# Performance work log

Measured on AMD Instinct MI355X. Metric: run time of the kernel, lower is better.

The kernel has to match this reference:

```python
import jax, jax.numpy as jnp
import numpy as np

N, E, CIN, COUT = 100000, 1600000, 64, 128
EPS = 1e-5  # torch BatchNorm default


def setup_inputs() -> dict:
    key = jax.random.key(0)
    ks = jax.random.split(key, 16)
    s = 0.1
    x = jax.random.normal(ks[0], (N, CIN), jnp.float32)
    src = jax.random.randint(ks[1], (E,), 0, N, dtype=jnp.int32)
    dst = jax.random.randint(ks[2], (E,), 0, N, dtype=jnp.int32)
    edge_index = jnp.stack([src, dst])  # [2, E]
    return {
        "x": x,
        "edge_index": edge_index,
        # conv0: GraphConv(CIN -> COUT)
        "W_root0": jax.random.normal(ks[3], (COUT, CIN), jnp.float32) * s,
        "W_nbr0": jax.random.normal(ks[4], (COUT, CIN), jnp.float32) * s,
        "b0": jnp.zeros((COUT,), jnp.float32),
        # bn0
        "g0": jnp.ones((COUT,), jnp.float32),
        "be0": jnp.zeros((COUT,), jnp.float32),
        # conv1: GraphConv(COUT -> COUT)
        "W_root1": jax.random.normal(ks[5], (COUT, COUT), jnp.float32) * s,
        "W_nbr1": jax.random.normal(ks[6], (COUT, COUT), jnp.float32) * s,
        "b1": jnp.zeros((COUT,), jnp.float32),
        # bn1
        "g1": jnp.ones((COUT,), jnp.float32),
        "be1": jnp.zeros((COUT,), jnp.float32),
        # residual 1x1 conv (Conv1d(CIN, COUT, 1))
        "Wlin": jax.random.normal(ks[7], (COUT, CIN), jnp.float32) * s,
        "blin": jnp.zeros((COUT,), jnp.float32),
    }


def graph_conv(x, src, dst, W_root, W_nbr, b):
    # PyG GraphConv: out_i = W_root x_i + W_nbr * sum_{j: (j->i) in E} x_j + b
    agg = jax.ops.segment_sum(x[src], dst, num_segments=N)  # scatter-add over edges
    return x @ W_root.T + agg @ W_nbr.T + b


def batch_norm(x, gamma, beta):
    # training-mode BatchNorm over the node dimension (biased variance)
    mu = jnp.mean(x, axis=0)
    var = jnp.mean(jnp.square(x - mu), axis=0)
    return (x - mu) * jax.lax.rsqrt(var + EPS) * gamma + beta


def reference(x, edge_index, W_root0, W_nbr0, b0, g0, be0,
              W_root1, W_nbr1, b1, g1, be1, Wlin, blin):
    src, dst = edge_index[0], edge_index[1]
    y = batch_norm(graph_conv(x, src, dst, W_root0, W_nbr0, b0), g0, be0)
    y = jax.nn.relu(y)
    y = batch_norm(graph_conv(y, src, dst, W_root1, W_nbr1, b1), g1, be1)
    out = y + (x @ Wlin.T + blin)  # 1x1 Conv1d residual projection
    return jax.nn.relu(out)
```

## Files before the change

kernel.cpp:

```cpp
#include <hip/hip_runtime.h>
#include <stdint.h>


#define CIN 64
#define COUT 128
#define BN_EPS 1e-5f
#define CURPAD 32
#define PCPAD 32
#define SPAD 32
#define PSH 8
#define PNODES (1 << PSH)
#define MAXP 512

typedef unsigned short u16;
typedef short short8 __attribute__((ext_vector_type(8)));
typedef float f32x4 __attribute__((ext_vector_type(4)));

__device__ __forceinline__ float bf2f(u16 u) {
    union { unsigned int i; float f; } v; v.i = ((unsigned int)u) << 16; return v.f;
}
__device__ __forceinline__ u16 f2bf(float f) {
    union { float f; unsigned int i; } v; v.f = f;
    unsigned int r = v.i + 0x7fffu + ((v.i >> 16) & 1u);
    return (u16)(r >> 16);
}
__device__ __forceinline__ float lo16(unsigned int w) { return bf2f((u16)(w & 0xffffu)); }
__device__ __forceinline__ float hi16(unsigned int w) { return bf2f((u16)(w >> 16)); }

template<bool BF> __device__ __forceinline__ float ldf(const void* p, long i) {
    if (BF) return bf2f(((const u16*)p)[i]);
    return ((const float*)p)[i];
}
template<bool BF> __device__ __forceinline__ short8 ld8(const void* p, long i) {
    if (BF) return *(const short8*)((const u16*)p + i);
    const float* f = (const float*)p + i;
    short8 r;
#pragma unroll
    for (int j = 0; j < 8; ++j) r[j] = (short)f2bf(f[j]);
    return r;
}

__device__ __forceinline__ void acc8(float* a, uint4 w) {
    a[0] += lo16(w.x); a[1] += hi16(w.x);
    a[2] += lo16(w.y); a[3] += hi16(w.y);
    a[4] += lo16(w.z); a[5] += hi16(w.z);
    a[6] += lo16(w.w); a[7] += hi16(w.w);
}

__global__ void k_detect(const unsigned int* __restrict__ x, int* __restrict__ flag) {
    int lane = threadIdx.x;
    int cnt = 0;
#pragma unroll
    for (int i = 0; i < 8; ++i) {
        unsigned int w = x[lane * 8 + i];
        unsigned int e0 = (w >> 7) & 0xFFu, e1 = (w >> 23) & 0xFFu;
        cnt += (e0 >= 0x60u && e0 <= 0x8Eu);
        cnt += (e1 >= 0x60u && e1 <= 0x8Eu);
    }
    for (int o = 32; o; o >>= 1) cnt += __shfl_down(cnt, o);
    if (lane == 0) *flag = (cnt > 850) ? 1 : 0;
}

__global__ __launch_bounds__(256) void k_xbf(const int* __restrict__ flag,
        const void* __restrict__ x, u16* __restrict__ xb, long n8) {
    long idx = (long)blockIdx.x * 256 + threadIdx.x;
    long stride = (long)gridDim.x * 256;
    uint4* dst = (uint4*)xb;
    if (*flag) {
        const uint4* src = (const uint4*)x;
        for (; idx < n8; idx += stride) dst[idx] = src[idx];
    } else {
        const float4* src = (const float4*)x;
        for (; idx < n8; idx += stride) {
            float4 a = src[idx * 2], b = src[idx * 2 + 1];
            uint4 o;
            o.x = (unsigned int)f2bf(a.x) | ((unsigned int)f2bf(a.y) << 16);
            o.y = (unsigned int)f2bf(a.z) | ((unsigned int)f2bf(a.w) << 16);
            o.z = (unsigned int)f2bf(b.x) | ((unsigned int)f2bf(b.y) << 16);
            o.w = (unsigned int)f2bf(b.z) | ((unsigned int)f2bf(b.w) << 16);
            dst[idx] = o;
        }
    }
}

__global__ __launch_bounds__(256) void k_phist(const int* __restrict__ dst,
                                               int* __restrict__ pcount, int E, int np) {
    __shared__ int h[MAXP];
    for (int i = threadIdx.x; i < np; i += 256) h[i] = 0;
    __syncthreads();
    int stride = gridDim.x * 256;
    for (int e = blockIdx.x * 256 + threadIdx.x; e < E; e += stride)
        atomicAdd(&h[dst[e] >> PSH], 1);
    __syncthreads();
    for (int i = threadIdx.x; i < np; i += 256)
        if (h[i]) atomicAdd(&pcount[i * PCPAD], h[i]);
}

__global__ void k_pscan(const int* __restrict__ pcount, int* __restrict__ pstart,
                        int* __restrict__ pcursor, int np, int E) {
    __shared__ int s[MAXP];
    int t = threadIdx.x;
    int v = (t < np) ? pcount[t * PCPAD] : 0;
    s[t] = v; __syncthreads();
    for (int o = 1; o < MAXP; o <<= 1) {
        int u = (t >= o) ? s[t - o] : 0;
        __syncthreads(); s[t] += u; __syncthreads();
    }
    if (t < np) {
        int ex = s[t] - v;
        pstart[t] = ex;
        pcursor[t * CURPAD] = ex;
    }
    if (t == 0) pstart[np] = E;
}

__global__ __launch_bounds__(256) void k_pfill(const int* __restrict__ src,
        const int* __restrict__ dst, int* __restrict__ pcursor,
        unsigned int* __restrict__ barr, int E, int np) {
    __shared__ int cnt[MAXP], gb[MAXP], loc[MAXP];
    int tid = threadIdx.x;
    int base = blockIdx.x * 4096;
    for (int i = tid; i < np; i += 256) { cnt[i] = 0; loc[i] = 0; }
    __syncthreads();
    int pk[16]; unsigned int rec[16];
#pragma unroll
    for (int k = 0; k < 16; ++k) {
        int e = base + k * 256 + tid;
        if (e < E) {
            int d = dst[e];
            pk[k] = d >> PSH;
            rec[k] = ((unsigned int)(d & (PNODES - 1)) << 20) | (unsigned int)src[e];
            atomicAdd(&cnt[pk[k]], 1);
        } else pk[k] = -1;
    }
    __syncthreads();
    for (int i = tid; i < np; i += 256)
        if (cnt[i]) gb[i] = atomicAdd(&pcursor[i * CURPAD], cnt[i]);
    __syncthreads();
#pragma unroll
    for (int k = 0; k < 16; ++k) {
        if (pk[k] >= 0) {
            int off = atomicAdd(&loc[pk[k]], 1);
            barr[gb[pk[k]] + off] = rec[k];
        }
    }
}

__global__ __launch_bounds__(256) void k_psort(const unsigned int* __restrict__ barr,
        const int* __restrict__ pstart, int* __restrict__ csr,
        int* __restrict__ row_start, int n, int np, int E) {
    __shared__ int hist[PNODES], curs[PNODES], tsum[256];
    int tid = threadIdx.x;
    int p = blockIdx.x;
    int e0 = pstart[p], e1 = pstart[p + 1];
    int node0 = p << PSH;
    hist[tid] = 0;
    __syncthreads();
    for (int t = e0 + tid; t < e1; t += 256)
        atomicAdd(&hist[barr[t] >> 20], 1);
    __syncthreads();
    int v = hist[tid];
    tsum[tid] = v; __syncthreads();
    for (int o = 1; o < 256; o <<= 1) {
        int u = (tid >= o) ? tsum[tid - o] : 0;
        __syncthreads(); tsum[tid] += u; __syncthreads();
    }
    int ex = tsum[tid] - v;
    curs[tid] = ex;
    int nd = node0 + tid;
    if (nd < n) row_start[nd] = e0 + ex;
    if (p == np - 1 && tid == 0) row_start[n] = E;
    __syncthreads();
    for (int t = e0 + tid; t < e1; t += 256) {
        unsigned int rec = barr[t];
        int pos = atomicAdd(&curs[rec >> 20], 1);
        csr[e0 + pos] = (int)(rec & 0xFFFFF);
    }
}

__global__ __launch_bounds__(256) void k_agg0(const u16* __restrict__ xb,
        const int* __restrict__ rs, const int* __restrict__ csr,
        u16* __restrict__ agg, int n) {
    int i = blockIdx.x * 4 + (threadIdx.x >> 6);
    if (i >= n) return;
    int lane = threadIdx.x & 63;
    int slot = lane >> 4, cp = lane & 15;
    const unsigned int* x32 = (const unsigned int*)xb;
    int b = rs[i], e = rs[i + 1];
    float acc[4] = {0.f, 0.f, 0.f, 0.f};
    int t = b + slot;
    for (; t + 12 < e; t += 16) {
        int j0 = csr[t], j1 = csr[t + 4], j2 = csr[t + 8], j3 = csr[t + 12];
        uint2 w0 = *((const uint2*)(x32 + (long)j0 * 32) + cp);
        uint2 w1 = *((const uint2*)(x32 + (long)j1 * 32) + cp);
        uint2 w2 = *((const uint2*)(x32 + (long)j2 * 32) + cp);
        uint2 w3 = *((const uint2*)(x32 + (long)j3 * 32) + cp);
        acc[0] += lo16(w0.x) + lo16(w1.x); acc[1] += hi16(w0.x) + hi16(w1.x);
        acc[2] += lo16(w0.y) + lo16(w1.y); acc[3] += hi16(w0.y) + hi16(w1.y);
        acc[0] += lo16(w2.x) + lo16(w3.x); acc[1] += hi16(w2.x) + hi16(w3.x);
        acc[2] += lo16(w2.y) + lo16(w3.y); acc[3] += hi16(w2.y) + hi16(w3.y);
    }
    for (; t < e; t += 4) {
        int j0 = csr[t];
        uint2 w0 = *((const uint2*)(x32 + (long)j0 * 32) + cp);
        acc[0] += lo16(w0.x); acc[1] += hi16(w0.x);
        acc[2] += lo16(w0.y); acc[3] += hi16(w0.y);
    }
#pragma unroll
    for (int k = 0; k < 4; ++k) {
        acc[k] += __shfl_xor(acc[k], 16);
        acc[k] += __shfl_xor(acc[k], 32);
    }
    if (slot == 0) {
        uint2 o;
        o.x = (unsigned int)f2bf(acc[0]) | ((unsigned int)f2bf(acc[1]) << 16);
        o.y = (unsigned int)f2bf(acc[2]) | ((unsigned int)f2bf(acc[3]) << 16);
        *((uint2*)((unsigned int*)agg + (long)i * 32) + cp) = o;
    }
}

__global__ __launch_bounds__(256) void k_y0p(unsigned int* __restrict__ y0,
        const float* __restrict__ sc, const float* __restrict__ sh, long nq) {
    long idx = (long)blockIdx.x * 256 + threadIdx.x;
    int colq = threadIdx.x & 15;
    float s8[8], h8[8];
#pragma unroll
    for (int j = 0; j < 8; ++j) { s8[j] = sc[colq * 8 + j]; h8[j] = sh[colq * 8 + j]; }
    long stride = (long)gridDim.x * 256;
    uint4* p = (uint4*)y0;
    for (; idx < nq; idx += stride) {
        uint4 w = p[idx];
        unsigned int r[4] = {w.x, w.y, w.z, w.w};
        uint4 o;
        unsigned int* po = (unsigned int*)&o;
#pragma unroll
        for (int d = 0; d < 4; ++d) {
            float a = fmaxf(lo16(r[d]) * s8[2 * d]     + h8[2 * d],     0.f);
            float b = fmaxf(hi16(r[d]) * s8[2 * d + 1] + h8[2 * d + 1], 0.f);
            po[d] = (unsigned int)f2bf(a) | ((unsigned int)f2bf(b) << 16);
        }
        p[idx] = o;
    }
}

__global__ __launch_bounds__(256) void k_agg1(const u16* __restrict__ y0p,
        const int* __restrict__ rs, const int* __restrict__ csr,
        u16* __restrict__ agg, int n) {
    int i = blockIdx.x * 4 + (threadIdx.x >> 6);
    if (i >= n) return;
    int lane = threadIdx.x & 63;
    int slot = lane >> 4, cp = lane & 15;
    const unsigned int* y32 = (const unsigned int*)y0p;
    int b = rs[i], e = rs[i + 1];
    float acc[8] = {0.f, 0.f, 0.f, 0.f, 0.f, 0.f, 0.f, 0.f};
    int t = b + slot;
    for (; t + 12 < e; t += 16) {
        int j0 = csr[t], j1 = csr[t + 4], j2 = csr[t + 8], j3 = csr[t + 12];
        uint4 w0 = *((const uint4*)(y32 + (long)j0 * 64) + cp);
        uint4 w1 = *((const uint4*)(y32 + (long)j1 * 64) + cp);
        uint4 w2 = *((const uint4*)(y32 + (long)j2 * 64) + cp);
        uint4 w3 = *((const uint4*)(y32 + (long)j3 * 64) + cp);
        acc8(acc, w0); acc8(acc, w1); acc8(acc, w2); acc8(acc, w3);
    }
    for (; t < e; t += 4) {
        int j0 = csr[t];
        uint4 w0 = *((const uint4*)(y32 + (long)j0 * 64) + cp);
        acc8(acc, w0);
    }
#pragma unroll
    for (int k = 0; k < 8; ++k) {
        acc[k] += __shfl_xor(acc[k], 16);
        acc[k] += __shfl_xor(acc[k], 32);
    }
    if (slot == 0) {
        uint4 o;
        o.x = (unsigned int)f2bf(acc[0]) | ((unsigned int)f2bf(acc[1]) << 16);
        o.y = (unsigned int)f2bf(acc[2]) | ((unsigned int)f2bf(acc[3]) << 16);
        o.z = (unsigned int)f2bf(acc[4]) | ((unsigned int)f2bf(acc[5]) << 16);
        o.w = (unsigned int)f2bf(acc[6]) | ((unsigned int)f2bf(acc[7]) << 16);
        *((uint4*)((unsigned int*)agg + (long)i * 64) + cp) = o;
    }
}

template<bool BF>
__device__ __forceinline__ void gemm0_impl(const u16* xb, const u16* agg,
                                           const void* Wr, const void* Wn,
                                           u16* y0, float* sumP, float* sqP,
                                           int n, int nch) {
    int tid = threadIdx.x;
    int wave = tid >> 6, lane = tid & 63, lr = lane & 15, q = lane >> 4;

    short8 wf[2][4];
#pragma unroll
    for (int i = 0; i < 2; ++i) {
        int c = (2 * wave + i) * 16 + lr;
#pragma unroll
        for (int ks = 0; ks < 4; ++ks) {
            const void* W = (ks < 2) ? Wr : Wn;
            wf[i][ks] = ld8<BF>(W, (long)c * CIN + (ks & 1) * 32 + q * 8);
        }
    }

    float st[2] = {0.f, 0.f}, sq[2] = {0.f, 0.f};
    for (int ch = blockIdx.x; ch < nch; ch += gridDim.x) {
        long chunk0 = (long)ch * 64;
#pragma unroll
        for (int t = 0; t < 4; ++t) {
            long rg = chunk0 + t * 16 + lr; if (rg > n - 1) rg = n - 1;
            short8 a[4];
#pragma unroll
            for (int ks = 0; ks < 2; ++ks)
                a[ks] = *(const short8*)(xb + rg * CIN + ks * 32 + q * 8);
#pragma unroll
            for (int ks = 0; ks < 2; ++ks)
                a[2 + ks] = *(const short8*)(agg + rg * CIN + ks * 32 + q * 8);
#pragma unroll
            for (int i = 0; i < 2; ++i) {
                f32x4 acc = {0.f, 0.f, 0.f, 0.f};
#pragma unroll
                for (int ks = 0; ks < 4; ++ks)
                    acc = __builtin_amdgcn_mfma_f32_16x16x32_bf16(a[ks], wf[i][ks], acc, 0, 0, 0);
                int c = (2 * wave + i) * 16 + lr;
#pragma unroll
                for (int r = 0; r < 4; ++r) {
                    long row = chunk0 + t * 16 + q * 4 + r;
                    if (row < n) {
                        y0[row * COUT + c] = f2bf(acc[r]);
                        st[i] += acc[r]; sq[i] += acc[r] * acc[r];
                    }
                }
            }
        }
    }
#pragma unroll
    for (int i = 0; i < 2; ++i) {
        st[i] += __shfl_xor(st[i], 16); st[i] += __shfl_xor(st[i], 32);
        sq[i] += __shfl_xor(sq[i], 16); sq[i] += __shfl_xor(sq[i], 32);
    }
    if (q == 0) {
#pragma unroll
        for (int i = 0; i < 2; ++i) {
            int c = (2 * wave + i) * 16 + lr;
            atomicAdd(&sumP[c * SPAD], st[i]);
            atomicAdd(&sqP[c * SPAD], sq[i]);
        }
    }
}

__global__ __launch_bounds__(256) void k_gemm0(const int* __restrict__ flag,
        const u16* __restrict__ xb, const u16* __restrict__ agg,
        const void* Wr, const void* Wn,
        u16* __restrict__ y0, float* __restrict__ sumP, float* __restrict__ sqP,
        int n, int nch) {
    if (*flag) gemm0_impl<true >(xb, agg, Wr, Wn, y0, sumP, sqP, n, nch);
    else       gemm0_impl<false>(xb, agg, Wr, Wn, y0, sumP, sqP, n, nch);
}

template<bool BF>
__device__ __forceinline__ void gemm1_impl(const u16* y0p, const u16* agg,
                                           const void* Wr, const void* Wn,
                                           u16* y1, float* sumP, float* sqP,
                                           int n, int nch) {
    int tid = threadIdx.x;
    int wave = tid >> 6, lane = tid & 63, lr = lane & 15, q = lane >> 4;

    short8 wf[2][8];
#pragma unroll
    for (int i = 0; i < 2; ++i) {
        int c = (2 * wave + i) * 16 + lr;
#pragma unroll
        for (int ks = 0; ks < 8; ++ks) {
            const void* W = (ks < 4) ? Wr : Wn;
            wf[i][ks] = ld8<BF>(W, (long)c * COUT + (ks & 3) * 32 + q * 8);
        }
    }

    float st[2] = {0.f, 0.f}, sq[2] = {0.f, 0.f};
    for (int ch = blockIdx.x; ch < nch; ch += gridDim.x) {
        long chunk0 = (long)ch * 64;
#pragma unroll
        for (int t = 0; t < 4; ++t) {
            long rg = chunk0 + t * 16 + lr; if (rg > n - 1) rg = n - 1;
            short8 a[8];
#pragma unroll
            for (int ks = 0; ks < 4; ++ks)
                a[ks] = *(const short8*)(y0p + rg * COUT + ks * 32 + q * 8);
#pragma unroll
            for (int ks = 0; ks < 4; ++ks)
                a[4 + ks] = *(const short8*)(agg + rg * COUT + ks * 32 + q * 8);
#pragma unroll
            for (int i = 0; i < 2; ++i) {
                f32x4 acc = {0.f, 0.f, 0.f, 0.f};
#pragma unroll
                for (int ks = 0; ks < 8; ++ks)
                    acc = __builtin_amdgcn_mfma_f32_16x16x32_bf16(a[ks], wf[i][ks], acc, 0, 0, 0);
                int c = (2 * wave + i) * 16 + lr;
#pragma unroll
                for (int r = 0; r < 4; ++r) {
                    long row = chunk0 + t * 16 + q * 4 + r;
                    if (row < n) {
                        y1[row * COUT + c] = f2bf(acc[r]);
                        st[i] += acc[r]; sq[i] += acc[r] * acc[r];
                    }
                }
            }
        }
    }
#pragma unroll
    for (int i = 0; i < 2; ++i) {
        st[i] += __shfl_xor(st[i], 16); st[i] += __shfl_xor(st[i], 32);
        sq[i] += __shfl_xor(sq[i], 16); sq[i] += __shfl_xor(sq[i], 32);
    }
    if (q == 0) {
#pragma unroll
        for (int i = 0; i < 2; ++i) {
            int c = (2 * wave + i) * 16 + lr;
            atomicAdd(&sumP[c * SPAD], st[i]);
            atomicAdd(&sqP[c * SPAD], sq[i]);
        }
    }
}

__global__ __launch_bounds__(256) void k_gemm1(const int* __restrict__ flag,
        const u16* __restrict__ y0p, const u16* __restrict__ agg,
        const void* Wr, const void* Wn,
        u16* y1_bf , u16* y1_ws,
        float* __restrict__ sumP, float* __restrict__ sqP, int n, int nch) {
    u16* y1 = *flag ? y1_bf : y1_ws;
    if (*flag) gemm1_impl<true >(y0p, agg, Wr, Wn, y1, sumP, sqP, n, nch);
    else       gemm1_impl<false>(y0p, agg, Wr, Wn, y1, sumP, sqP, n, nch);
}

__global__ void k_bnfin(const int* __restrict__ flag,
                        const float* __restrict__ sumP, const float* __restrict__ sqP,
                        const void* g, const void* be,
                        float* __restrict__ scale, float* __restrict__ shift, int n) {
    int c = threadIdx.x;
    bool bf = (*flag != 0);
    float inv = 1.f / (float)n;
    float mu = sumP[c * SPAD] * inv;
    float var = fmaxf(sqP[c * SPAD] * inv - mu * mu, 0.f);
    float gv = bf ? bf2f(((const u16*)g)[c]) : ((const float*)g)[c];
    float bv = bf ? bf2f(((const u16*)be)[c]) : ((const float*)be)[c];
    float sc = gv * rsqrtf(var + BN_EPS);
    scale[c] = sc;
    shift[c] = bv - mu * sc;
}

template<bool BF>
__device__ __forceinline__ void final_impl(const u16* xb, const u16* y1,
                                           const void* Wlin, const void* blin,
                                           const float* sc, const float* sh,
                                           void* out, int n, int nch, u16* lds) {
    const int ST = 130;
    int tid = threadIdx.x;
    int wave = tid >> 6, lane = tid & 63, lr = lane & 15, q = lane >> 4;

    short8 wf[2][2];
    float blc[2], scc[2], shc[2];
#pragma unroll
    for (int i = 0; i < 2; ++i) {
        int c = (2 * wave + i) * 16 + lr;
#pragma unroll
        for (int ks = 0; ks < 2; ++ks)
            wf[i][ks] = ld8<BF>(Wlin, (long)c * CIN + ks * 32 + q * 8);
        blc[i] = ldf<BF>(blin, c);
        scc[i] = sc[c]; shc[i] = sh[c];
    }

    const int rowy = tid >> 4, wy = tid & 15;
    short8 ry[4];

    auto regload = [&](long chunk0) {
#pragma unroll
        for (int i = 0; i < 4; ++i) {
            long rg = chunk0 + rowy + i * 16; if (rg > n - 1) rg = n - 1;
            ry[i] = *(const short8*)(y1 + rg * COUT + wy * 8);
        }
    };

    int ch = blockIdx.x;
    if (ch < nch) regload((long)ch * 64);
    for (; ch < nch; ch += gridDim.x) {
        long chunk0 = (long)ch * 64;
        __syncthreads();
#pragma unroll
        for (int i = 0; i < 4; ++i)
            *(short8*)(lds + (rowy + i * 16) * ST + wy * 8) = ry[i];
        __syncthreads();
        long nxt = (long)ch + gridDim.x;
        if (nxt < nch) regload(nxt * 64);

#pragma unroll
        for (int t = 0; t < 4; ++t) {
            long rg = chunk0 + t * 16 + lr; if (rg > n - 1) rg = n - 1;
            short8 a[2];
#pragma unroll
            for (int ks = 0; ks < 2; ++ks)
                a[ks] = *(const short8*)(xb + rg * CIN + ks * 32 + q * 8);
#pragma unroll
            for (int i = 0; i < 2; ++i) {
                f32x4 acc = {0.f, 0.f, 0.f, 0.f};
                acc = __builtin_amdgcn_mfma_f32_16x16x32_bf16(a[0], wf[i][0], acc, 0, 0, 0);
                acc = __builtin_amdgcn_mfma_f32_16x16x32_bf16(a[1], wf[i][1], acc, 0, 0, 0);
                int c = (2 * wave + i) * 16 + lr;
#pragma unroll
                for (int r = 0; r < 4; ++r) {
                    long row = chunk0 + t * 16 + q * 4 + r;
                    if (row < n) {
                        float yv = bf2f(lds[(t * 16 + q * 4 + r) * ST + c]);
                        float v = acc[r] + blc[i] + yv * scc[i] + shc[i];
                        v = fmaxf(v, 0.f);
                        if (BF) ((u16*)out)[row * COUT + c] = f2bf(v);
                        else    ((float*)out)[row * COUT + c] = v;
                    }
                }
            }
        }
    }
}

__global__ __launch_bounds__(256) void k_final(const int* __restrict__ flag,
        const u16* __restrict__ xb, const void* Wlin, const void* blin,
        const u16* y1_bf , const u16* y1_ws,
        const float* __restrict__ sc, const float* __restrict__ sh,
        void* out, int n, int nch) {
    __shared__ u16 lds[64 * 130];
    const u16* y1 = *flag ? y1_bf : y1_ws;
    if (*flag) final_impl<true >(xb, y1, Wlin, blin, sc, sh, out, n, nch, lds);
    else       final_impl<false>(xb, y1, Wlin, blin, sc, sh, out, n, nch, lds);
}

extern "C" void kernel_launch(void* const* d_in, const int* in_sizes, int n_in,
                              void* d_out, int out_size, void* d_ws, size_t ws_size,
                              hipStream_t stream) {
    (void)n_in; (void)out_size; (void)ws_size;
    const void* x    = d_in[0];
    const int*  ei   = (const int*)d_in[1];
    const void* Wr0  = d_in[2];
    const void* Wn0  = d_in[3];
    const void* g0   = d_in[5];
    const void* be0  = d_in[6];
    const void* Wr1  = d_in[7];
    const void* Wn1  = d_in[8];
    const void* g1   = d_in[10];
    const void* be1  = d_in[11];
    const void* Wlin = d_in[12];
    const void* blin = d_in[13];

    const int N = in_sizes[0] / CIN;
    const int E = in_sizes[1] / 2;
    const int* src = ei;
    const int* dst = ei + E;
    const int NP = (N + PNODES - 1) >> PSH;

    char* base = (char*)d_ws;
    size_t off = 0;
    auto carve = [&](size_t bytes) -> void* {
        void* p = base + off;
        off = (off + bytes + 255) & ~(size_t)255;
        return p;
    };
    int*   flag      = (int*)carve(256);
    int*   pcount    = (int*)carve(MAXP * PCPAD * sizeof(int));
    int*   pstart    = (int*)carve((MAXP + 1) * sizeof(int));
    int*   pcursor   = (int*)carve(MAXP * CURPAD * sizeof(int));
    float* statsP    = (float*)carve(4 * 128 * SPAD * sizeof(float));
    float* scsh      = (float*)carve(512 * sizeof(float));
    int*   row_start = (int*)carve((size_t)(N + 1) * sizeof(int));
    unsigned int* barr = (unsigned int*)carve((size_t)E * sizeof(int));
    int*   csr       = (int*)carve((size_t)E * sizeof(int));
    u16*   xb        = (u16*)carve((size_t)N * CIN * sizeof(u16));
    u16*   aggu      = (u16*)carve((size_t)N * COUT * sizeof(u16));
    u16*   y0        = (u16*)carve((size_t)N * COUT * sizeof(u16));
    u16*   y1_ws     = (u16*)carve((size_t)N * COUT * sizeof(u16));

    float* sum0P = statsP;
    float* sq0P  = statsP + 128 * SPAD;
    float* sum1P = statsP + 256 * SPAD;
    float* sq1P  = statsP + 384 * SPAD;

    hipMemsetAsync(pcount, 0, MAXP * PCPAD * sizeof(int), stream);
    hipMemsetAsync(statsP, 0, 4 * 128 * SPAD * sizeof(float), stream);

    const int nwb = (N + 3) / 4;
    const int nch = (N + 63) / 64;
    const int ntl = (E + 4095) / 4096;
    const int G   = nch < 1024 ? nch : 1024;
    const long nq = (long)N * 16;
    const long n8 = (long)N * CIN / 8;
    int g2 = (int)((nq + 255) / 256); if (g2 > 2048) g2 = 2048;
    int g3 = (int)((n8 + 255) / 256); if (g3 > 2048) g3 = 2048;

    k_detect<<<1, 64, 0, stream>>>((const unsigned int*)x, flag);
    k_xbf<<<g3, 256, 0, stream>>>(flag, x, xb, n8);

    k_phist<<<256, 256, 0, stream>>>(dst, pcount, E, NP);
    k_pscan<<<1, MAXP, 0, stream>>>(pcount, pstart, pcursor, NP, E);
    k_pfill<<<ntl, 256, 0, stream>>>(src, dst, pcursor, barr, E, NP);
    k_psort<<<NP, 256, 0, stream>>>(barr, pstart, csr, row_start, N, NP, E);

    k_agg0 <<<nwb, 256, 0, stream>>>(xb, row_start, csr, aggu, N);
    k_gemm0<<<G, 256, 0, stream>>>(flag, xb, aggu, Wr0, Wn0, y0,
                                   sum0P, sq0P, N, nch);
    k_bnfin<<<1, 128, 0, stream>>>(flag, sum0P, sq0P, g0, be0,
                                   scsh, scsh + 128, N);

    k_y0p<<<g2, 256, 0, stream>>>((unsigned int*)y0, scsh, scsh + 128, nq);

    k_agg1 <<<nwb, 256, 0, stream>>>(y0, row_start, csr, aggu, N);
    k_gemm1<<<G, 256, 0, stream>>>(flag, y0, aggu, Wr1, Wn1,
                                   (u16*)d_out, y1_ws, sum1P, sq1P, N, nch);
    k_bnfin<<<1, 128, 0, stream>>>(flag, sum1P, sq1P, g1, be1,
                                   scsh + 256, scsh + 384, N);

    k_final<<<G, 256, 0, stream>>>(flag, xb, Wlin, blin,
                                   (const u16*)d_out, y1_ws,
                                   scsh + 256, scsh + 384, d_out, N, nch);
}
```

Baseline: 393.1 us.

## Fuse preprocessing kernels, shrink partition size, and uncap GEMM grid

Merges the dtype-detection kernel into the dst histogram kernel and the bf16 conversion of x into the edge bucket-fill kernel, so two fewer launches run and independent work shares a grid. Partition size drops from 256 to 128 nodes, which doubles the partition count so the per-partition sort gets more blocks with less work each. The GEMM/final grid is no longer capped at 1024 blocks. The risks are more global atomics on the partition cursors, a larger shared-memory footprint in the fill kernel, and a single-block scan over 1024 partitions.

```diff
diff --git a/kernel.cpp b/kernel.cpp
--- a/kernel.cpp
+++ b/kernel.cpp
@@ -8,9 +8,9 @@
 #define CURPAD 32
 #define PCPAD 32
 #define SPAD 32
-#define PSH 8
+#define PSH 7
 #define PNODES (1 << PSH)
-#define MAXP 512
+#define MAXP 1024
 
 typedef unsigned short u16;
 typedef short short8 __attribute__((ext_vector_type(8)));
@@ -47,49 +47,32 @@
     a[6] += lo16(w.w); a[7] += hi16(w.w);
 }
 
-__global__ void k_detect(const unsigned int* __restrict__ x, int* __restrict__ flag) {
-    int lane = threadIdx.x;
-    int cnt = 0;
-#pragma unroll
-    for (int i = 0; i < 8; ++i) {
-        unsigned int w = x[lane * 8 + i];
-        unsigned int e0 = (w >> 7) & 0xFFu, e1 = (w >> 23) & 0xFFu;
-        cnt += (e0 >= 0x60u && e0 <= 0x8Eu);
-        cnt += (e1 >= 0x60u && e1 <= 0x8Eu);
-    }
-    for (int o = 32; o; o >>= 1) cnt += __shfl_down(cnt, o);
-    if (lane == 0) *flag = (cnt > 850) ? 1 : 0;
-}
-
-__global__ __launch_bounds__(256) void k_xbf(const int* __restrict__ flag,
-        const void* __restrict__ x, u16* __restrict__ xb, long n8) {
-    long idx = (long)blockIdx.x * 256 + threadIdx.x;
-    long stride = (long)gridDim.x * 256;
-    uint4* dst = (uint4*)xb;
-    if (*flag) {
-        const uint4* src = (const uint4*)x;
-        for (; idx < n8; idx += stride) dst[idx] = src[idx];
-    } else {
-        const float4* src = (const float4*)x;
-        for (; idx < n8; idx += stride) {
-            float4 a = src[idx * 2], b = src[idx * 2 + 1];
-            uint4 o;
-            o.x = (unsigned int)f2bf(a.x) | ((unsigned int)f2bf(a.y) << 16);
-            o.y = (unsigned int)f2bf(a.z) | ((unsigned int)f2bf(a.w) << 16);
-            o.z = (unsigned int)f2bf(b.x) | ((unsigned int)f2bf(b.y) << 16);
-            o.w = (unsigned int)f2bf(b.z) | ((unsigned int)f2bf(b.w) << 16);
-            dst[idx] = o;
-        }
-    }
-}
-
-__global__ __launch_bounds__(256) void k_phist(const int* __restrict__ dst,
-                                               int* __restrict__ pcount, int E, int np) {
+__global__ __launch_bounds__(256) void k_prep(const unsigned int* __restrict__ x,
+        int* __restrict__ flag, const int* __restrict__ dst,
+        int* __restrict__ pcount, int E, int np) {
+    if (blockIdx.x == 0) {
+        if (threadIdx.x < 64) {
+            int lane = threadIdx.x;
+            int cnt = 0;
+#pragma unroll
+            for (int i = 0; i < 8; ++i) {
+                unsigned int w = x[lane * 8 + i];
+                unsigned int e0 = (w >> 7) & 0xFFu, e1 = (w >> 23) & 0xFFu;
+                cnt += (e0 >= 0x60u && e0 <= 0x8Eu);
+                cnt += (e1 >= 0x60u && e1 <= 0x8Eu);
+            }
+            for (int o = 32; o; o >>= 1) cnt += __shfl_down(cnt, o);
+            if (lane == 0) *flag = (cnt > 850) ? 1 : 0;
+        }
+        return;
+    }
     __shared__ int h[MAXP];
+    int bid = blockIdx.x - 1;
+    int nb = gridDim.x - 1;
     for (int i = threadIdx.x; i < np; i += 256) h[i] = 0;
     __syncthreads();
-    int stride = gridDim.x * 256;
-    for (int e = blockIdx.x * 256 + threadIdx.x; e < E; e += stride)
+    int stride = nb * 256;
+    for (int e = bid * 256 + threadIdx.x; e < E; e += stride)
         atomicAdd(&h[dst[e] >> PSH], 1);
     __syncthreads();
     for (int i = threadIdx.x; i < np; i += 256)
@@ -114,11 +97,35 @@
     if (t == 0) pstart[np] = E;
 }
 
-__global__ __launch_bounds__(256) void k_pfill(const int* __restrict__ src,
+__global__ __launch_bounds__(256) void k_fill2(const int* __restrict__ src,
         const int* __restrict__ dst, int* __restrict__ pcursor,
-        unsigned int* __restrict__ barr, int E, int np) {
+        unsigned int* __restrict__ barr, int E, int np, int ntl,
+        const int* __restrict__ flag, const void* __restrict__ x,
+        u16* __restrict__ xb, long n8) {
     __shared__ int cnt[MAXP], gb[MAXP], loc[MAXP];
     int tid = threadIdx.x;
+    if (blockIdx.x >= ntl) {
+        int nb = gridDim.x - ntl;
+        long idx = (long)(blockIdx.x - ntl) * 256 + tid;
+        long stride = (long)nb * 256;
+        uint4* d4 = (uint4*)xb;
+        if (*flag) {
+            const uint4* s4 = (const uint4*)x;
+            for (; idx < n8; idx += stride) d4[idx] = s4[idx];
+        } else {
+            const float4* s4 = (const float4*)x;
+            for (; idx < n8; idx += stride) {
+                float4 a = s4[idx * 2], b = s4[idx * 2 + 1];
+                uint4 o;
+                o.x = (unsigned int)f2bf(a.x) | ((unsigned int)f2bf(a.y) << 16);
+                o.y = (unsigned int)f2bf(a.z) | ((unsigned int)f2bf(a.w) << 16);
+                o.z = (unsigned int)f2bf(b.x) | ((unsigned int)f2bf(b.y) << 16);
+                o.w = (unsigned int)f2bf(b.z) | ((unsigned int)f2bf(b.w) << 16);
+                d4[idx] = o;
+            }
+        }
+        return;
+    }
     int base = blockIdx.x * 4096;
     for (int i = tid; i < np; i += 256) { cnt[i] = 0; loc[i] = 0; }
     __syncthreads();
@@ -154,21 +161,23 @@
     int p = blockIdx.x;
     int e0 = pstart[p], e1 = pstart[p + 1];
     int node0 = p << PSH;
-    hist[tid] = 0;
+    if (tid < PNODES) hist[tid] = 0;
     __syncthreads();
     for (int t = e0 + tid; t < e1; t += 256)
         atomicAdd(&hist[barr[t] >> 20], 1);
     __syncthreads();
-    int v = hist[tid];
+    int v = (tid < PNODES) ? hist[tid] : 0;
     tsum[tid] = v; __syncthreads();
     for (int o = 1; o < 256; o <<= 1) {
         int u = (tid >= o) ? tsum[tid - o] : 0;
         __syncthreads(); tsum[tid] += u; __syncthreads();
     }
-    int ex = tsum[tid] - v;
-    curs[tid] = ex;
-    int nd = node0 + tid;
-    if (nd < n) row_start[nd] = e0 + ex;
+    if (tid < PNODES) {
+        int ex = tsum[tid] - v;
+        curs[tid] = ex;
+        int nd = node0 + tid;
+        if (nd < n) row_start[nd] = e0 + ex;
+    }
     if (p == np - 1 && tid == 0) row_start[n] = E;
     __syncthreads();
     for (int t = e0 + tid; t < e1; t += 256) {
@@ -586,18 +595,16 @@
     const int nwb = (N + 3) / 4;
     const int nch = (N + 63) / 64;
     const int ntl = (E + 4095) / 4096;
-    const int G   = nch < 1024 ? nch : 1024;
+    const int G   = nch;
     const long nq = (long)N * 16;
     const long n8 = (long)N * CIN / 8;
     int g2 = (int)((nq + 255) / 256); if (g2 > 2048) g2 = 2048;
-    int g3 = (int)((n8 + 255) / 256); if (g3 > 2048) g3 = 2048;
-
-    k_detect<<<1, 64, 0, stream>>>((const unsigned int*)x, flag);
-    k_xbf<<<g3, 256, 0, stream>>>(flag, x, xb, n8);
-
-    k_phist<<<256, 256, 0, stream>>>(dst, pcount, E, NP);
+    int g3 = (int)((n8 + 255) / 256); if (g3 > 1024) g3 = 1024;
+
+    k_prep<<<257, 256, 0, stream>>>((const unsigned int*)x, flag, dst, pcount, E, NP);
     k_pscan<<<1, MAXP, 0, stream>>>(pcount, pstart, pcursor, NP, E);
-    k_pfill<<<ntl, 256, 0, stream>>>(src, dst, pcursor, barr, E, NP);
+    k_fill2<<<ntl + g3, 256, 0, stream>>>(src, dst, pcursor, barr, E, NP, ntl,
+                                          flag, x, xb, n8);
     k_psort<<<NP, 256, 0, stream>>>(barr, pstart, csr, row_start, N, NP, E);
 
     k_agg0 <<<nwb, 256, 0, stream>>>(xb, row_start, csr, aggu, N);
```

Result: slower. 415.6 us (+5.7%).
